# Optimization experiments

Measured on AMD Instinct MI355X. Metric: run time of the kernel, lower is better.

The kernel has to match this reference:

```python
import jax, jax.numpy as jnp
import numpy as np

IDIM1, IDIM2, HDIM = 512, 512, 256
EPS = 1e-5

def _layernorm(x, g, b):
    mu = jnp.mean(x, axis=-1, keepdims=True)
    var = jnp.var(x, axis=-1, keepdims=True)
    return (x - mu) * jax.lax.rsqrt(var + EPS) * g + b

def setup_inputs() -> dict:
    key = jax.random.key(0)
    ks = jax.random.split(key, 8)
    B, N, T = 16, 32, 256
    s1 = 1.0 / np.sqrt(IDIM1)
    s2 = 1.0 / np.sqrt(IDIM2)
    s3 = 1.0 / np.sqrt(HDIM)
    return {
        "x1": jax.random.normal(ks[0], (B, N, IDIM1), jnp.float32),
        "x2": jax.random.normal(ks[1], (B, T, IDIM2), jnp.float32),
        "W1": jax.random.uniform(ks[2], (IDIM1, HDIM), jnp.float32, -s1, s1),
        "b1": jax.random.uniform(ks[3], (HDIM,), jnp.float32, -s1, s1),
        "W2": jax.random.uniform(ks[4], (IDIM2, HDIM), jnp.float32, -s2, s2),
        "b2": jax.random.uniform(ks[5], (HDIM,), jnp.float32, -s2, s2),
        "W3": jax.random.uniform(ks[6], (HDIM, HDIM), jnp.float32, -s3, s3),
        "b3": jax.random.uniform(ks[7], (HDIM,), jnp.float32, -s3, s3),
        "g_norm": jnp.ones((HDIM,), jnp.float32),
        "be_norm": jnp.zeros((HDIM,), jnp.float32),
        "g_norm1": jnp.ones((HDIM,), jnp.float32),
        "be_norm1": jnp.zeros((HDIM,), jnp.float32),
    }

def reference(x1, x2, W1, b1, W2, b2, W3, b3, g_norm, be_norm, g_norm1, be_norm1):
    h1 = jax.nn.relu(x1 @ W1 + b1)          # [B,N,H]
    h2 = jax.nn.relu(x2 @ W2 + b2)          # [B,T,H]
    x = h1[:, :, None, :] * h2[:, None, :, :]  # [B,N,T,H] broadcast Hadamard
    x = _layernorm(x, g_norm, be_norm)
    x = x @ W3 + b3
    return jax.nn.relu(_layernorm(x, g_norm1, be_norm1))
```

## Files before the change

### kernel.cpp

```cpp
#include <hip/hip_runtime.h>
#include <hip/hip_bf16.h>
#include <stdint.h>

#define BB 16
#define NN 32
#define TT 256
#define HH 256
#define DD 512
#define EPSF 1e-5f

#define TROWS 32
#define ROWB  512

typedef __attribute__((ext_vector_type(8))) short short8;
typedef __attribute__((ext_vector_type(4))) float floatx4;

__device__ __forceinline__ unsigned short f2bf(float f) {
    union { float f; unsigned u; } v; v.f = f;
    unsigned u = v.u;
    unsigned r = u + 0x7FFFu + ((u >> 16) & 1u);
    return (unsigned short)(r >> 16);
}
__device__ __forceinline__ float bf2f(unsigned short h) {
    union { unsigned u; float f; } v; v.u = ((unsigned)h) << 16;
    return v.f;
}

__device__ __forceinline__ void split2(float f0, float f1, unsigned& hp, unsigned& lp) {
    union { float f; unsigned u; } a0, a1, r0, r1;
    a0.f = f0; a1.f = f1;
    const unsigned h0 = a0.u & 0xFFFF0000u;
    const unsigned h1 = a1.u & 0xFFFF0000u;
    union { unsigned u; float f; } b0, b1;
    b0.u = h0; b1.u = h1;
    r0.f = f0 - b0.f;
    r1.f = f1 - b1.f;
    hp = (a0.u >> 16) | h1;
    lp = (r0.u >> 16) | (r1.u & 0xFFFF0000u);
}

__global__ __launch_bounds__(256) void prep_kernel(
    const float* __restrict__ x1, const float* __restrict__ x2,
    const float* __restrict__ W1, const float* __restrict__ b1,
    const float* __restrict__ W2, const float* __restrict__ b2,
    const float* __restrict__ W3,
    float* __restrict__ h1, float* __restrict__ h2,
    unsigned short* __restrict__ W3p_hi, unsigned short* __restrict__ W3p_lo)
{
    const int blk = blockIdx.x;
    const int tid = threadIdx.x;

    if (blk >= 1152) {
        const int p  = (blk - 1152) * 256 + tid;
        const int o0 = p * 16;
        unsigned short thi[16], tlo[16];
#pragma unroll
        for (int e = 0; e < 16; ++e) {
            const int o    = o0 + e;
            const int j    = o & 7;
            const int lane = (o >> 3) & 63;
            const int kk   = (o >> 9) & 7;
            const int ct   = o >> 12;
            const int krow = kk * 32 + (lane >> 4) * 8 + j;
            const int col  = ct * 16 + (lane & 15);
            const float w  = W3[krow * HH + col];
            const unsigned short hi = f2bf(w);
            thi[e] = hi;
            tlo[e] = f2bf(w - bf2f(hi));
        }
        unsigned wh[8], wl[8];
#pragma unroll
        for (int e = 0; e < 8; ++e) {
            wh[e] = (unsigned)thi[2 * e] | ((unsigned)thi[2 * e + 1] << 16);
            wl[e] = (unsigned)tlo[2 * e] | ((unsigned)tlo[2 * e + 1] << 16);
        }
        uint4* dh = reinterpret_cast<uint4*>(W3p_hi + o0);
        dh[0] = make_uint4(wh[0], wh[1], wh[2], wh[3]);
        dh[1] = make_uint4(wh[4], wh[5], wh[6], wh[7]);
        uint4* dl = reinterpret_cast<uint4*>(W3p_lo + o0);
        dl[0] = make_uint4(wl[0], wl[1], wl[2], wl[3]);
        dl[1] = make_uint4(wl[4], wl[5], wl[6], wl[7]);
        return;
    }

    __shared__ float xs[8][DD];

    const int rowgrp  = blk >> 1;
    const int colbase = (blk & 1) * 128;

    const float* x; const float* W; const float* bias; float* h; int row0;
    if (rowgrp < 64) { x = x1; W = W1; bias = b1; h = h1; row0 = rowgrp * 8; }
    else             { x = x2; W = W2; bias = b2; h = h2; row0 = (rowgrp - 64) * 8; }

    {
        const float4* xg = reinterpret_cast<const float4*>(x + (size_t)row0 * DD);
        float4* xl = reinterpret_cast<float4*>(&xs[0][0]);
#pragma unroll
        for (int i = 0; i < 4; ++i) xl[tid + 256 * i] = xg[tid + 256 * i];
    }
    __syncthreads();

    const int jj  = tid & 127;
    const int rh  = tid >> 7;
    const int col = colbase + jj;

    float acc[4] = {0.0f, 0.0f, 0.0f, 0.0f};
    const float* Wp = W + col;

    for (int k = 0; k < DD; k += 8) {
        float w[8];
#pragma unroll
        for (int q = 0; q < 8; ++q) w[q] = Wp[(size_t)(k + q) * HH];
#pragma unroll
        for (int r = 0; r < 4; ++r) {
            const float4 xa = *reinterpret_cast<const float4*>(&xs[rh * 4 + r][k]);
            const float4 xb = *reinterpret_cast<const float4*>(&xs[rh * 4 + r][k + 4]);
            float s = acc[r];
            s = fmaf(xa.x, w[0], s); s = fmaf(xa.y, w[1], s);
            s = fmaf(xa.z, w[2], s); s = fmaf(xa.w, w[3], s);
            s = fmaf(xb.x, w[4], s); s = fmaf(xb.y, w[5], s);
            s = fmaf(xb.z, w[6], s); s = fmaf(xb.w, w[7], s);
            acc[r] = s;
        }
    }

    const float bb = bias[col];
#pragma unroll
    for (int r = 0; r < 4; ++r) {
        const float v = acc[r] + bb;
        h[(size_t)(row0 + rh * 4 + r) * HH + col] = v > 0.0f ? v : 0.0f;
    }
}

__global__ __launch_bounds__(256) void fused_mfma_kernel(
    const float* __restrict__ h1, const float* __restrict__ h2,
    const unsigned short* __restrict__ W3p_hi,
    const unsigned short* __restrict__ W3p_lo,
    const float* __restrict__ b3,
    const float* __restrict__ g0, const float* __restrict__ be0,
    const float* __restrict__ g1, const float* __restrict__ be1,
    float* __restrict__ out)
{
    __shared__ __align__(16) unsigned short Ah_s[TROWS * 256];
    __shared__ __align__(16) unsigned short Al_s[TROWS * 256];

    const int tid  = threadIdx.x;
    const int wave = tid >> 6;
    const int lane = tid & 63;
    const int blk  = blockIdx.x;
    const int tile = blk & 7;
    const int n    = (blk >> 3) & 31;
    const int b    = blk >> 8;

    {
        const float* h1row = h1 + ((size_t)b * NN + n) * HH;
        const float4 h1v  = *reinterpret_cast<const float4*>(h1row + 4 * lane);
        const float4 g0v  = *reinterpret_cast<const float4*>(g0  + 4 * lane);
        const float4 be0v = *reinterpret_cast<const float4*>(be0 + 4 * lane);
        const float* h2b  = h2 + ((size_t)b * TT + tile * TROWS) * HH;

#pragma unroll
        for (int half = 0; half < 2; ++half) {
            float4 v[4]; float s[4], q[4];
#pragma unroll
            for (int i = 0; i < 4; ++i) {
                const int r = wave * 8 + half * 4 + i;
                v[i] = *reinterpret_cast<const float4*>(h2b + (size_t)r * HH + 4 * lane);
                v[i].x *= h1v.x; v[i].y *= h1v.y; v[i].z *= h1v.z; v[i].w *= h1v.w;
                s[i] = v[i].x + v[i].y + v[i].z + v[i].w;
                q[i] = v[i].x * v[i].x + v[i].y * v[i].y
                     + v[i].z * v[i].z + v[i].w * v[i].w;
            }
#pragma unroll
            for (int off = 32; off >= 1; off >>= 1) {
#pragma unroll
                for (int i = 0; i < 4; ++i) {
                    s[i] += __shfl_xor(s[i], off, 64);
                    q[i] += __shfl_xor(q[i], off, 64);
                }
            }
#pragma unroll
            for (int i = 0; i < 4; ++i) {
                const int r = wave * 8 + half * 4 + i;
                const float mu  = s[i] * (1.0f / HH);
                const float var = q[i] * (1.0f / HH) - mu * mu;
                const float rs  = rsqrtf(var + EPSF);
                float af0 = (v[i].x - mu) * rs * g0v.x + be0v.x;
                float af1 = (v[i].y - mu) * rs * g0v.y + be0v.y;
                float af2 = (v[i].z - mu) * rs * g0v.z + be0v.z;
                float af3 = (v[i].w - mu) * rs * g0v.w + be0v.w;
                unsigned hp0, lp0, hp1, lp1;
                split2(af0, af1, hp0, lp0);
                split2(af2, af3, hp1, lp1);
                const int byteoff = (lane * 8) ^ ((r & 7) << 4);
                *reinterpret_cast<uint2*>(
                    reinterpret_cast<char*>(Ah_s) + r * ROWB + byteoff)
                    = make_uint2(hp0, hp1);
                *reinterpret_cast<uint2*>(
                    reinterpret_cast<char*>(Al_s) + r * ROWB + byteoff)
                    = make_uint2(lp0, lp1);
            }
        }
    }
    __syncthreads();

    const int m  = lane & 15;
    const int qd = lane >> 4;

    floatx4 acc[2][4];
#pragma unroll
    for (int ct = 0; ct < 4; ++ct) {
        const float bv = b3[wave * 64 + ct * 16 + m];
#pragma unroll
        for (int rt = 0; rt < 2; ++rt) {
            acc[rt][ct][0] = bv; acc[rt][ct][1] = bv;
            acc[rt][ct][2] = bv; acc[rt][ct][3] = bv;
        }
    }

    const char* AhB = reinterpret_cast<const char*>(Ah_s);
    const char* AlB = reinterpret_cast<const char*>(Al_s);

#pragma unroll 2
    for (int kk = 0; kk < 8; ++kk) {
        short8 bh[4], bl[4];
#pragma unroll
        for (int ct = 0; ct < 4; ++ct) {
            const size_t off = ((size_t)((wave * 4 + ct) * 8 + kk) * 64 + lane) * 8;
            bh[ct] = *reinterpret_cast<const short8*>(W3p_hi + off);
            bl[ct] = *reinterpret_cast<const short8*>(W3p_lo + off);
        }
        const int swzoff = (kk * 64 + qd * 16) ^ ((m & 7) << 4);
#pragma unroll
        for (int rt = 0; rt < 2; ++rt) {
            const int rowbyte = (rt * 16 + m) * ROWB;
            const short8 ah = *reinterpret_cast<const short8*>(AhB + rowbyte + swzoff);
            const short8 al = *reinterpret_cast<const short8*>(AlB + rowbyte + swzoff);
#pragma unroll
            for (int ct = 0; ct < 4; ++ct) {
                floatx4 c = acc[rt][ct];
                c = __builtin_amdgcn_mfma_f32_16x16x32_bf16(ah, bh[ct], c, 0, 0, 0);
                c = __builtin_amdgcn_mfma_f32_16x16x32_bf16(al, bh[ct], c, 0, 0, 0);
                c = __builtin_amdgcn_mfma_f32_16x16x32_bf16(ah, bl[ct], c, 0, 0, 0);
                acc[rt][ct] = c;
            }
        }
    }

    float ssum[8], qsum[8];
    {
#pragma unroll
        for (int rt = 0; rt < 2; ++rt)
#pragma unroll
            for (int reg = 0; reg < 4; ++reg) {
                float s = 0.0f, q = 0.0f;
#pragma unroll
                for (int ct = 0; ct < 4; ++ct) {
                    const float y = acc[rt][ct][reg];
                    s += y; q = fmaf(y, y, q);
                }
                ssum[rt * 4 + reg] = s; qsum[rt * 4 + reg] = q;
            }
#pragma unroll
        for (int off = 1; off < 16; off <<= 1) {
#pragma unroll
            for (int e = 0; e < 8; ++e) {
                ssum[e] += __shfl_xor(ssum[e], off, 64);
                qsum[e] += __shfl_xor(qsum[e], off, 64);
            }
        }
    }

    __syncthreads();
    float2* Spart = reinterpret_cast<float2*>(Ah_s);
    float2* LNP   = reinterpret_cast<float2*>(Al_s);

    if (m == 0) {
#pragma unroll
        for (int rt = 0; rt < 2; ++rt)
#pragma unroll
            for (int reg = 0; reg < 4; ++reg) {
                const int row = rt * 16 + qd * 4 + reg;
                Spart[row * 4 + wave] = make_float2(ssum[rt * 4 + reg], qsum[rt * 4 + reg]);
            }
    }
    __syncthreads();

    if (tid < TROWS) {
        float s = 0.0f, q = 0.0f;
#pragma unroll
        for (int w = 0; w < 4; ++w) {
            const float2 p = Spart[tid * 4 + w];
            s += p.x; q += p.y;
        }
        const float mu  = s * (1.0f / HH);
        const float var = q * (1.0f / HH) - mu * mu;
        LNP[tid] = make_float2(mu, rsqrtf(var + EPSF));
    }
    __syncthreads();

    {
        const int colb = wave * 64;
        float g1c[4], be1c[4];
#pragma unroll
        for (int ct = 0; ct < 4; ++ct) {
            g1c[ct]  = g1[colb + ct * 16 + m];
            be1c[ct] = be1[colb + ct * 16 + m];
        }
        float* outb = out + (((size_t)b * NN + n) * TT + tile * TROWS) * HH;

#pragma unroll
        for (int rt = 0; rt < 2; ++rt)
#pragma unroll
            for (int reg = 0; reg < 4; ++reg) {
                const int row = rt * 16 + qd * 4 + reg;
                const float2 p = LNP[row];
#pragma unroll
                for (int ct = 0; ct < 4; ++ct) {
                    const float y = acc[rt][ct][reg];
                    const float o = fmaxf((y - p.x) * p.y * g1c[ct] + be1c[ct], 0.0f);
                    outb[(size_t)row * HH + colb + ct * 16 + m] = o;
                }
            }
    }
}

extern "C" void kernel_launch(void* const* d_in, const int* in_sizes, int n_in,
                              void* d_out, int out_size, void* d_ws, size_t ws_size,
                              hipStream_t stream) {
    const float* x1  = (const float*)d_in[0];
    const float* x2  = (const float*)d_in[1];
    const float* W1  = (const float*)d_in[2];
    const float* b1  = (const float*)d_in[3];
    const float* W2  = (const float*)d_in[4];
    const float* b2  = (const float*)d_in[5];
    const float* W3  = (const float*)d_in[6];
    const float* b3  = (const float*)d_in[7];
    const float* g0  = (const float*)d_in[8];
    const float* be0 = (const float*)d_in[9];
    const float* g1  = (const float*)d_in[10];
    const float* be1 = (const float*)d_in[11];
    float* out = (float*)d_out;

    float* h1 = (float*)d_ws;
    float* h2 = h1 + (size_t)BB * NN * HH;
    unsigned short* W3p_hi = (unsigned short*)(h2 + (size_t)BB * TT * HH);
    unsigned short* W3p_lo = W3p_hi + (size_t)HH * HH;

    hipLaunchKernelGGL(prep_kernel, dim3(1168), dim3(256), 0, stream,
                       x1, x2, W1, b1, W2, b2, W3, h1, h2, W3p_hi, W3p_lo);

    hipLaunchKernelGGL(fused_mfma_kernel, dim3(4096), dim3(256), 0, stream,
                       h1, h2, W3p_hi, W3p_lo, b3, g0, be0, g1, be1, out);
}
```

Baseline: 252.1 us.

## Fold first layernorm affine into W3 and precompute row stats in separate kernel

Folds the first layernorm's gamma into W3 and its beta plus b3 into a precomputed bias vector c2. The per-row rsqrt is applied after the MFMA accumulation instead of before. Row mean and rstd come from a new stats kernel, so the fused kernel only subtracts the mean before splitting to bf16 hi/lo. Cross-lane reductions switch from shfl_xor to DPP row adds. The cost is an extra kernel launch, a second read of h2, and a new stats buffer in global memory.

```diff
diff --git a/kernel.cpp b/kernel.cpp
--- a/kernel.cpp
+++ b/kernel.cpp
@@ -39,16 +39,39 @@
     lp = (r0.u >> 16) | (r1.u & 0xFFFF0000u);
 }
 
+template <int CTRL>
+__device__ __forceinline__ float dpp_add(float x) {
+    const int t = __builtin_amdgcn_update_dpp(
+        0, __float_as_int(x), CTRL, 0xF, 0xF, true);
+    return x + __int_as_float(t);
+}
+template <int CTRL>
+__device__ __forceinline__ void dpp_stage8(float* s, float* q) {
+#pragma unroll
+    for (int i = 0; i < 4; ++i) { s[i] = dpp_add<CTRL>(s[i]); q[i] = dpp_add<CTRL>(q[i]); }
+}
+
 __global__ __launch_bounds__(256) void prep_kernel(
     const float* __restrict__ x1, const float* __restrict__ x2,
     const float* __restrict__ W1, const float* __restrict__ b1,
     const float* __restrict__ W2, const float* __restrict__ b2,
-    const float* __restrict__ W3,
+    const float* __restrict__ W3, const float* __restrict__ b3,
+    const float* __restrict__ g0, const float* __restrict__ be0,
     float* __restrict__ h1, float* __restrict__ h2,
-    unsigned short* __restrict__ W3p_hi, unsigned short* __restrict__ W3p_lo)
+    unsigned short* __restrict__ W3p_hi, unsigned short* __restrict__ W3p_lo,
+    float* __restrict__ c2)
 {
     const int blk = blockIdx.x;
     const int tid = threadIdx.x;
+
+    if (blk == 1168) {
+        const int j = tid;
+        float acc = b3[j];
+        for (int k = 0; k < HH; ++k)
+            acc = fmaf(be0[k], W3[k * HH + j], acc);
+        c2[j] = acc;
+        return;
+    }
 
     if (blk >= 1152) {
         const int p  = (blk - 1152) * 256 + tid;
@@ -63,7 +86,7 @@
             const int ct   = o >> 12;
             const int krow = kk * 32 + (lane >> 4) * 8 + j;
             const int col  = ct * 16 + (lane & 15);
-            const float w  = W3[krow * HH + col];
+            const float w  = W3[krow * HH + col] * g0[krow];
             const unsigned short hi = f2bf(w);
             thi[e] = hi;
             tlo[e] = f2bf(w - bf2f(hi));
@@ -132,12 +155,54 @@
     }
 }
 
+__global__ __launch_bounds__(256) void stats_kernel(
+    const float* __restrict__ h1, const float* __restrict__ h2,
+    float2* __restrict__ stats)
+{
+    const int tid  = threadIdx.x;
+    const int wave = tid >> 6;
+    const int lane = tid & 63;
+    const int bn   = blockIdx.x;
+    const int b    = bn >> 5;
+
+    const float4 h1v = *reinterpret_cast<const float4*>(
+        h1 + (size_t)bn * HH + 4 * lane);
+    const float* h2b = h2 + (size_t)b * TT * HH;
+    float2* srow = stats + (size_t)bn * TT;
+
+    for (int batch = 0; batch < 16; ++batch) {
+        float s[4], q[4];
+#pragma unroll
+        for (int i = 0; i < 4; ++i) {
+            const int r = batch * 16 + wave * 4 + i;
+            float4 v = *reinterpret_cast<const float4*>(h2b + (size_t)r * HH + 4 * lane);
+            v.x *= h1v.x; v.y *= h1v.y; v.z *= h1v.z; v.w *= h1v.w;
+            s[i] = v.x + v.y + v.z + v.w;
+            q[i] = v.x * v.x + v.y * v.y + v.z * v.z + v.w * v.w;
+        }
+        dpp_stage8<0x111>(s, q);
+        dpp_stage8<0x112>(s, q);
+        dpp_stage8<0x114>(s, q);
+        dpp_stage8<0x118>(s, q);
+        dpp_stage8<0x142>(s, q);
+        dpp_stage8<0x143>(s, q);
+        if (lane == 63) {
+#pragma unroll
+            for (int i = 0; i < 4; ++i) {
+                const int r = batch * 16 + wave * 4 + i;
+                const float mu  = s[i] * (1.0f / HH);
+                const float var = q[i] * (1.0f / HH) - mu * mu;
+                srow[r] = make_float2(mu, rsqrtf(var + EPSF));
+            }
+        }
+    }
+}
+
 __global__ __launch_bounds__(256) void fused_mfma_kernel(
     const float* __restrict__ h1, const float* __restrict__ h2,
     const unsigned short* __restrict__ W3p_hi,
     const unsigned short* __restrict__ W3p_lo,
-    const float* __restrict__ b3,
-    const float* __restrict__ g0, const float* __restrict__ be0,
+    const float2* __restrict__ stats, const float* __restrict__ c2,
     const float* __restrict__ g1, const float* __restrict__ be1,
     float* __restrict__ out)
 {
@@ -152,46 +217,27 @@
     const int n    = (blk >> 3) & 31;
     const int b    = blk >> 8;
 
+    const float2* statrow = stats + ((size_t)(b * NN + n) * TT + tile * TROWS);
+
     {
         const float* h1row = h1 + ((size_t)b * NN + n) * HH;
         const float4 h1v  = *reinterpret_cast<const float4*>(h1row + 4 * lane);
-        const float4 g0v  = *reinterpret_cast<const float4*>(g0  + 4 * lane);
-        const float4 be0v = *reinterpret_cast<const float4*>(be0 + 4 * lane);
         const float* h2b  = h2 + ((size_t)b * TT + tile * TROWS) * HH;
 
 #pragma unroll
         for (int half = 0; half < 2; ++half) {
-            float4 v[4]; float s[4], q[4];
 #pragma unroll
             for (int i = 0; i < 4; ++i) {
                 const int r = wave * 8 + half * 4 + i;
-                v[i] = *reinterpret_cast<const float4*>(h2b + (size_t)r * HH + 4 * lane);
-                v[i].x *= h1v.x; v[i].y *= h1v.y; v[i].z *= h1v.z; v[i].w *= h1v.w;
-                s[i] = v[i].x + v[i].y + v[i].z + v[i].w;
-                q[i] = v[i].x * v[i].x + v[i].y * v[i].y
-                     + v[i].z * v[i].z + v[i].w * v[i].w;
-            }
-#pragma unroll
-            for (int off = 32; off >= 1; off >>= 1) {
-#pragma unroll
-                for (int i = 0; i < 4; ++i) {
-                    s[i] += __shfl_xor(s[i], off, 64);
-                    q[i] += __shfl_xor(q[i], off, 64);
-                }
-            }
-#pragma unroll
-            for (int i = 0; i < 4; ++i) {
-                const int r = wave * 8 + half * 4 + i;
-                const float mu  = s[i] * (1.0f / HH);
-                const float var = q[i] * (1.0f / HH) - mu * mu;
-                const float rs  = rsqrtf(var + EPSF);
-                float af0 = (v[i].x - mu) * rs * g0v.x + be0v.x;
-                float af1 = (v[i].y - mu) * rs * g0v.y + be0v.y;
-                float af2 = (v[i].z - mu) * rs * g0v.z + be0v.z;
-                float af3 = (v[i].w - mu) * rs * g0v.w + be0v.w;
+                float4 v = *reinterpret_cast<const float4*>(h2b + (size_t)r * HH + 4 * lane);
+                const float mu = statrow[r].x;
+                float a0 = fmaf(v.x, h1v.x, -mu);
+                float a1 = fmaf(v.y, h1v.y, -mu);
+                float a2 = fmaf(v.z, h1v.z, -mu);
+                float a3 = fmaf(v.w, h1v.w, -mu);
                 unsigned hp0, lp0, hp1, lp1;
-                split2(af0, af1, hp0, lp0);
-                split2(af2, af3, hp1, lp1);
+                split2(a0, a1, hp0, lp0);
+                split2(a2, a3, hp1, lp1);
                 const int byteoff = (lane * 8) ^ ((r & 7) << 4);
                 *reinterpret_cast<uint2*>(
                     reinterpret_cast<char*>(Ah_s) + r * ROWB + byteoff)
@@ -209,14 +255,12 @@
 
     floatx4 acc[2][4];
 #pragma unroll
-    for (int ct = 0; ct < 4; ++ct) {
-        const float bv = b3[wave * 64 + ct * 16 + m];
+    for (int ct = 0; ct < 4; ++ct)
 #pragma unroll
         for (int rt = 0; rt < 2; ++rt) {
-            acc[rt][ct][0] = bv; acc[rt][ct][1] = bv;
-            acc[rt][ct][2] = bv; acc[rt][ct][3] = bv;
-        }
-    }
+            acc[rt][ct][0] = 0.0f; acc[rt][ct][1] = 0.0f;
+            acc[rt][ct][2] = 0.0f; acc[rt][ct][3] = 0.0f;
+        }
 
     const char* AhB = reinterpret_cast<const char*>(Ah_s);
     const char* AlB = reinterpret_cast<const char*>(Al_s);
@@ -247,6 +291,21 @@
         }
     }
 
+    {
+        float c2c[4];
+#pragma unroll
+        for (int ct = 0; ct < 4; ++ct) c2c[ct] = c2[wave * 64 + ct * 16 + m];
+#pragma unroll
+        for (int rt = 0; rt < 2; ++rt)
+#pragma unroll
+            for (int reg = 0; reg < 4; ++reg) {
+                const float rs = statrow[rt * 16 + qd * 4 + reg].y;
+#pragma unroll
+                for (int ct = 0; ct < 4; ++ct)
+                    acc[rt][ct][reg] = fmaf(rs, acc[rt][ct][reg], c2c[ct]);
+            }
+    }
+
     float ssum[8], qsum[8];
     {
 #pragma unroll
@@ -261,21 +320,17 @@
                 }
                 ssum[rt * 4 + reg] = s; qsum[rt * 4 + reg] = q;
             }
-#pragma unroll
-        for (int off = 1; off < 16; off <<= 1) {
-#pragma unroll
-            for (int e = 0; e < 8; ++e) {
-                ssum[e] += __shfl_xor(ssum[e], off, 64);
-                qsum[e] += __shfl_xor(qsum[e], off, 64);
-            }
-        }
+        dpp_stage8<0x111>(ssum, qsum); dpp_stage8<0x111>(ssum + 4, qsum + 4);
+        dpp_stage8<0x112>(ssum, qsum); dpp_stage8<0x112>(ssum + 4, qsum + 4);
+        dpp_stage8<0x114>(ssum, qsum); dpp_stage8<0x114>(ssum + 4, qsum + 4);
+        dpp_stage8<0x118>(ssum, qsum); dpp_stage8<0x118>(ssum + 4, qsum + 4);
     }
 
     __syncthreads();
     float2* Spart = reinterpret_cast<float2*>(Ah_s);
     float2* LNP   = reinterpret_cast<float2*>(Al_s);
 
-    if (m == 0) {
+    if (m == 15) {
 #pragma unroll
         for (int rt = 0; rt < 2; ++rt)
 #pragma unroll
@@ -346,10 +401,16 @@
     float* h2 = h1 + (size_t)BB * NN * HH;
     unsigned short* W3p_hi = (unsigned short*)(h2 + (size_t)BB * TT * HH);
     unsigned short* W3p_lo = W3p_hi + (size_t)HH * HH;
-
-    hipLaunchKernelGGL(prep_kernel, dim3(1168), dim3(256), 0, stream,
-                       x1, x2, W1, b1, W2, b2, W3, h1, h2, W3p_hi, W3p_lo);
+    float2* stats = (float2*)(W3p_lo + (size_t)HH * HH);
+    float* c2 = (float*)(stats + (size_t)BB * NN * TT);
+
+    hipLaunchKernelGGL(prep_kernel, dim3(1169), dim3(256), 0, stream,
+                       x1, x2, W1, b1, W2, b2, W3, b3, g0, be0,
+                       h1, h2, W3p_hi, W3p_lo, c2);
+
+    hipLaunchKernelGGL(stats_kernel, dim3(BB * NN), dim3(256), 0, stream,
+                       h1, h2, stats);
 
     hipLaunchKernelGGL(fused_mfma_kernel, dim3(4096), dim3(256), 0, stream,
-                       h1, h2, W3p_hi, W3p_lo, b3, g0, be0, g1, be1, out);
-}
+                       h1, h2, W3p_hi, W3p_lo, stats, c2, g1, be1, out);
+}
```

Measured after the change: 256.7 us. Within noise of the previous version (+1.8%).
